# Kernel tuning notes

Measured on AMD Instinct MI355X. Metric: run time of the kernel, lower is better.

Reference implementation:

```python
import jax, jax.numpy as jnp
import numpy as np

EMBED_DIM = 1024
NUM_HEADS = 16
HEAD_DIM = EMBED_DIM // NUM_HEADS
SCALE = HEAD_DIM ** -0.5


def setup_inputs() -> dict:
    key = jax.random.key(0)
    ks = jax.random.split(key, 5)
    B, N, D = 2, 2048, EMBED_DIM
    std = D ** -0.5
    x = jax.random.normal(ks[0], (B, N, D), dtype=jnp.float32)
    W_qkv = jax.random.normal(ks[1], (D, 3 * D), dtype=jnp.float32) * std
    b_qkv = jnp.zeros((3 * D,), dtype=jnp.float32)
    W_proj = jax.random.normal(ks[2], (D, D), dtype=jnp.float32) * std
    b_proj = jnp.zeros((D,), dtype=jnp.float32)
    return {"x": x, "W_qkv": W_qkv, "b_qkv": b_qkv, "W_proj": W_proj, "b_proj": b_proj}


def reference(x, W_qkv, b_qkv, W_proj, b_proj):
    B, N, D = x.shape
    H, Hd = NUM_HEADS, HEAD_DIM
    qkv = x @ W_qkv + b_qkv                      # (B, N, 3D)
    qkv = qkv.reshape(B, N, 3, H, Hd)
    q = qkv[:, :, 0].transpose(0, 2, 1, 3)       # (B, H, N, Hd)
    k = qkv[:, :, 1].transpose(0, 2, 1, 3)
    v = qkv[:, :, 2].transpose(0, 2, 1, 3)
    attn = jnp.einsum('bhqd,bhkd->bhqk', q, k) * SCALE  # (B, H, N, N)
    attn = jax.nn.softmax(attn, axis=-1)
    out = jnp.einsum('bhqk,bhkd->bhqd', attn, v)        # (B, H, N, Hd)
    out = out.transpose(0, 2, 1, 3).reshape(B, N, D)
    return out @ W_proj + b_proj
```

## Files before the change

### kernel.cpp

```cpp
#include <hip/hip_runtime.h>
#include <stdint.h>

#define BATCH 2
#define NH 16
#define SEQ 2048
#define DIM 1024
#define HD 64
#define MROWS (BATCH*SEQ)

typedef __attribute__((ext_vector_type(8))) _Float16 f16x8;
typedef __attribute__((ext_vector_type(16))) float f32x16;
typedef __attribute__((ext_vector_type(4))) float f32x4;
typedef __attribute__((ext_vector_type(2))) __fp16 fp16x2;
typedef __attribute__((ext_vector_type(4))) short short4v;

__device__ __forceinline__ short f2h(float f) {
  union { _Float16 h; short s; } u;
  u.h = (_Float16)f;
  return u.s;
}

__device__ __forceinline__ float fast_exp2(float x) {
#if __has_builtin(__builtin_amdgcn_exp2f)
  return __builtin_amdgcn_exp2f(x);
#else
  return exp2f(x);
#endif
}

__device__ __forceinline__ unsigned pk2(float a, float b) {
  union { fp16x2 h; unsigned u; } x;
  x.h = __builtin_amdgcn_cvt_pkrtz(a, b);
  return x.u;
}

__device__ __forceinline__ void perm32swap(unsigned &a, unsigned &b) {
  unsigned as = (unsigned)__shfl_xor((int)a, 32);
  unsigned bs = (unsigned)__shfl_xor((int)b, 32);
  bool lo = ((threadIdx.x & 63) < 32);
  unsigned na = lo ? a : bs;
  unsigned nb = lo ? as : b;
  a = na; b = nb;
}

__device__ __forceinline__ void async_load16(const void* g, void* l) {
  __builtin_amdgcn_global_load_lds((const __attribute__((address_space(1))) void*)g,
                                   (__attribute__((address_space(3))) void*)l, 16, 0, 0);
}

__global__ __launch_bounds__(256) void k_cvt(const float* __restrict__ in,
                                             short* __restrict__ out, int n4) {
  int i = blockIdx.x * 256 + threadIdx.x;
  if (i >= n4) return;
  float4 v = ((const float4*)in)[i];
  short4v o;
  o[0] = f2h(v.x); o[1] = f2h(v.y); o[2] = f2h(v.z); o[3] = f2h(v.w);
  ((short4v*)out)[i] = o;
}

__global__ __launch_bounds__(256) void k_transpose(const float* __restrict__ in,
                                                   short* __restrict__ out,
                                                   int K, int N) {
  __shared__ float t[32][33];
  int n0 = blockIdx.x * 32, k0 = blockIdx.y * 32;
  int tx = threadIdx.x, ty = threadIdx.y;
  #pragma unroll
  for (int i = 0; i < 32; i += 8)
    t[ty + i][tx] = in[(size_t)(k0 + ty + i) * N + (n0 + tx)];
  __syncthreads();
  #pragma unroll
  for (int i = 0; i < 32; i += 8)
    out[(size_t)(n0 + ty + i) * K + (k0 + tx)] = f2h(t[tx][ty + i]);
}

template <int MODE>
__global__ __launch_bounds__(256) void k_gemm_bt(
    const short* __restrict__ A, const short* __restrict__ Bt,
    const float* __restrict__ bias,
    short* __restrict__ Qd, short* __restrict__ Kd, short* __restrict__ Vtd,
    float* __restrict__ Cf, int Ncols, int Kdim) {
  constexpr int BM = 128, BN = 128, BK = 32;
  __shared__ short Al[BM * BK];
  __shared__ short Bl[BN * BK];
  const int tid = threadIdx.x;
  const int lane = tid & 63;
  const int wid = tid >> 6;
  const int wr = wid >> 1, wc = wid & 1;
  const int m0 = blockIdx.y * BM, n0 = blockIdx.x * BN;
  const int l15 = lane & 15, lk = (lane >> 4) * 8;

  f32x4 acc[4][4] = {};

  for (int k0 = 0; k0 < Kdim; k0 += BK) {
    __syncthreads();
    #pragma unroll
    for (int i = 0; i < 2; i++) {
      int c = i * 256 + tid;
      async_load16(A + (size_t)(m0 + (c >> 2)) * Kdim + k0 + (c & 3) * 8, &Al[c * 8]);
    }
    #pragma unroll
    for (int i = 0; i < 2; i++) {
      int c = i * 256 + tid;
      async_load16(Bt + (size_t)(n0 + (c >> 2)) * Kdim + k0 + (c & 3) * 8, &Bl[c * 8]);
    }
    __syncthreads();

    f16x8 af[4], bfr[4];
    #pragma unroll
    for (int i = 0; i < 4; i++)
      af[i] = *(const f16x8*)&Al[(wr * 64 + i * 16 + l15) * BK + lk];
    #pragma unroll
    for (int j = 0; j < 4; j++)
      bfr[j] = *(const f16x8*)&Bl[(wc * 64 + j * 16 + l15) * BK + lk];
    #pragma unroll
    for (int i = 0; i < 4; i++)
      #pragma unroll
      for (int j = 0; j < 4; j++)
        acc[i][j] = __builtin_amdgcn_mfma_f32_16x16x32_f16(af[i], bfr[j], acc[i][j], 0, 0, 0);
  }

  const int rl = (lane >> 4) * 4;
  if (MODE == 0) {
    #pragma unroll
    for (int j = 0; j < 4; j++) {
      int col = n0 + wc * 64 + j * 16 + l15;
      float bv = bias[col];
      int sec = col >> 10;
      int cc = col & 1023;
      int h = cc >> 6, hd = cc & 63;
      float mul = (sec == 0) ? (0.125f * 1.44269504088896f) : 1.0f;
      #pragma unroll
      for (int i = 0; i < 4; i++) {
        int rowb = m0 + wr * 64 + i * 16 + rl;
        #pragma unroll
        for (int r = 0; r < 4; r++) {
          int row = rowb + r;
          int b = row >> 11, nr = row & 2047;
          short v = f2h((acc[i][j][r] + bv) * mul);
          size_t bh = (size_t)(b * NH + h);
          size_t base2 = bh * (size_t)(SEQ * HD);
          if (sec == 0) {
            Qd[base2 + (size_t)nr * HD + hd] = v;
          } else if (sec == 1) {
            Kd[base2 + (size_t)(((nr >> 5) * 4 + (hd >> 4)) * 512 +
                                (((hd >> 3) & 1) * 32 + (nr & 31)) * 8 + (hd & 7))] = v;
          } else {
            Vtd[base2 + (size_t)(((nr >> 4) * 2 + (hd >> 5)) * 512 +
                                 (((nr >> 3) & 1) * 32 + (hd & 31)) * 8 + (nr & 7))] = v;
          }
        }
      }
    }
  } else {
    #pragma unroll
    for (int j = 0; j < 4; j++) {
      int col = n0 + wc * 64 + j * 16 + l15;
      float bv = bias[col];
      #pragma unroll
      for (int i = 0; i < 4; i++) {
        int rowb = m0 + wr * 64 + i * 16 + rl;
        #pragma unroll
        for (int r = 0; r < 4; r++)
          Cf[(size_t)(rowb + r) * Ncols + col] = acc[i][j][r] + bv;
      }
    }
  }
}

#define QBLK 256
#define NKVT (SEQ / 64)

#define PACK8(sv, R0, lsv, OUT) do {                                        \
    float e0_ = fast_exp2((sv)[R0 + 0]), e1_ = fast_exp2((sv)[R0 + 1]);     \
    float e2_ = fast_exp2((sv)[R0 + 2]), e3_ = fast_exp2((sv)[R0 + 3]);     \
    float e4_ = fast_exp2((sv)[R0 + 4]), e5_ = fast_exp2((sv)[R0 + 5]);     \
    float e6_ = fast_exp2((sv)[R0 + 6]), e7_ = fast_exp2((sv)[R0 + 7]);     \
    lsv += ((e0_ + e1_) + (e2_ + e3_)) + ((e4_ + e5_) + (e6_ + e7_));       \
    unsigned u0_ = pk2(e0_, e1_), u1_ = pk2(e2_, e3_);                      \
    unsigned u2_ = pk2(e4_, e5_), u3_ = pk2(e6_, e7_);                      \
    perm32swap(u0_, u2_);                                                   \
    perm32swap(u1_, u3_);                                                   \
    union { unsigned u[4]; f16x8 v; } W_;                                   \
    W_.u[0] = u0_; W_.u[1] = u1_; W_.u[2] = u2_; W_.u[3] = u3_;             \
    OUT = W_.v;                                                             \
  } while (0)

__global__ __launch_bounds__(256) void k_flash(const short* __restrict__ Qd,
                                               const short* __restrict__ KB,
                                               const short* __restrict__ VB,
                                               short* __restrict__ Od) {
  __shared__ short Kl[2][4096];
  __shared__ short Vl[2][4096];
  const int tid = threadIdx.x;
  const int lane = tid & 63;
  const int w = tid >> 6;
  const int l31 = lane & 31, lh = lane >> 5;
  const int bh = blockIdx.x;
  const int q0 = blockIdx.y * QBLK + w * 64;
  const size_t base = (size_t)bh * (size_t)(SEQ * HD);

  f16x8 qf[2][4];
  #pragma unroll
  for (int qt = 0; qt < 2; qt++)
    #pragma unroll
    for (int ds = 0; ds < 4; ds++)
      qf[qt][ds] = *(const f16x8*)(Qd + base + (size_t)(q0 + qt * 32 + l31) * HD +
                                   ds * 16 + lh * 8);

  f32x16 o[2][2] = {};
  float lsum0 = 0.f, lsum1 = 0.f;

#define STAGE(kvt, buf) do {                                                \
    const short* ks_ = KB + base + (size_t)(kvt) * 4096;                    \
    const short* vs_ = VB + base + (size_t)(kvt) * 4096;                    \
    async_load16(ks_ + tid * 8, &Kl[buf][tid * 8]);                         \
    async_load16(ks_ + (tid + 256) * 8, &Kl[buf][(tid + 256) * 8]);         \
    async_load16(vs_ + tid * 8, &Vl[buf][tid * 8]);                         \
    async_load16(vs_ + (tid + 256) * 8, &Vl[buf][(tid + 256) * 8]);         \
  } while (0)

  auto compute = [&](int cur) {
    f16x8 p0[4], p1[4];
    {
      f16x8 kf[4];
      #pragma unroll
      for (int ds = 0; ds < 4; ds++)
        kf[ds] = *(const f16x8*)&Kl[cur][(ds * 64 + lane) * 8];
      f32x16 sA0 = {}, sA1 = {};
      #pragma unroll
      for (int ds = 0; ds < 4; ds++) {
        sA0 = __builtin_amdgcn_mfma_f32_32x32x16_f16(kf[ds], qf[0][ds], sA0, 0, 0, 0);
        sA1 = __builtin_amdgcn_mfma_f32_32x32x16_f16(kf[ds], qf[1][ds], sA1, 0, 0, 0);
      }
      PACK8(sA0, 0, lsum0, p0[0]); PACK8(sA0, 8, lsum0, p0[1]);
      PACK8(sA1, 0, lsum1, p1[0]); PACK8(sA1, 8, lsum1, p1[1]);
    }
    {
      f16x8 kf[4];
      #pragma unroll
      for (int ds = 0; ds < 4; ds++)
        kf[ds] = *(const f16x8*)&Kl[cur][((4 + ds) * 64 + lane) * 8];
      f32x16 sB0 = {}, sB1 = {};
      #pragma unroll
      for (int ds = 0; ds < 4; ds++) {
        sB0 = __builtin_amdgcn_mfma_f32_32x32x16_f16(kf[ds], qf[0][ds], sB0, 0, 0, 0);
        sB1 = __builtin_amdgcn_mfma_f32_32x32x16_f16(kf[ds], qf[1][ds], sB1, 0, 0, 0);
      }
      PACK8(sB0, 0, lsum0, p0[2]); PACK8(sB0, 8, lsum0, p0[3]);
      PACK8(sB1, 0, lsum1, p1[2]); PACK8(sB1, 8, lsum1, p1[3]);
    }
    f16x8 vf[4][2];
    #pragma unroll
    for (int ks = 0; ks < 4; ks++)
      #pragma unroll
      for (int hdt = 0; hdt < 2; hdt++)
        vf[ks][hdt] = *(const f16x8*)&Vl[cur][((ks * 2 + hdt) * 64 + lane) * 8];
    #pragma unroll
    for (int ks = 0; ks < 4; ks++) {
      o[0][0] = __builtin_amdgcn_mfma_f32_32x32x16_f16(p0[ks], vf[ks][0], o[0][0], 0, 0, 0);
      o[0][1] = __builtin_amdgcn_mfma_f32_32x32x16_f16(p0[ks], vf[ks][1], o[0][1], 0, 0, 0);
      o[1][0] = __builtin_amdgcn_mfma_f32_32x32x16_f16(p1[ks], vf[ks][0], o[1][0], 0, 0, 0);
      o[1][1] = __builtin_amdgcn_mfma_f32_32x32x16_f16(p1[ks], vf[ks][1], o[1][1], 0, 0, 0);
    }
  };

  STAGE(0, 0);
  __syncthreads();
  for (int kvt = 0; kvt < NKVT; kvt++) {
    int cur = kvt & 1;
    if (kvt + 1 < NKVT) STAGE(kvt + 1, cur ^ 1);
    compute(cur);
    __syncthreads();
  }
#undef STAGE

  lsum0 += __shfl_xor(lsum0, 32);
  lsum1 += __shfl_xor(lsum1, 32);
  float inv0 = 1.f / lsum0, inv1 = 1.f / lsum1;

  const int b = bh >> 4, h = bh & 15;
  #pragma unroll
  for (int reg = 0; reg < 16; reg++) {
    int qrow = (reg & 3) + 8 * (reg >> 2) + 4 * lh;
    float s0 = __shfl(inv0, qrow);
    float s1 = __shfl(inv1, qrow);
    size_t r0 = (size_t)(b * SEQ + q0 + qrow) * DIM + h * 64;
    size_t r1 = (size_t)(b * SEQ + q0 + 32 + qrow) * DIM + h * 64;
    Od[r0 + l31]      = f2h(o[0][0][reg] * s0);
    Od[r0 + 32 + l31] = f2h(o[0][1][reg] * s0);
    Od[r1 + l31]      = f2h(o[1][0][reg] * s1);
    Od[r1 + 32 + l31] = f2h(o[1][1][reg] * s1);
  }
}

extern "C" void kernel_launch(void* const* d_in, const int* in_sizes, int n_in,
                              void* d_out, int out_size, void* d_ws, size_t ws_size,
                              hipStream_t stream) {
  const float* x     = (const float*)d_in[0];
  const float* Wqkv  = (const float*)d_in[1];
  const float* bqkv  = (const float*)d_in[2];
  const float* Wproj = (const float*)d_in[3];
  const float* bproj = (const float*)d_in[4];
  float* out = (float*)d_out;

  char* ws = (char*)d_ws;
  short* x_h    = (short*)(ws);
  short* Wqkv_t = (short*)(ws + ((size_t)8  << 20));
  short* Wproj_t= (short*)(ws + ((size_t)14 << 20));
  short* Qd     = (short*)(ws + ((size_t)16 << 20));
  short* Kd     = (short*)(ws + ((size_t)24 << 20));
  short* Vtd    = (short*)(ws + ((size_t)32 << 20));
  short* Od     = (short*)(ws + ((size_t)40 << 20));

  k_cvt<<<(MROWS * DIM / 4 + 255) / 256, 256, 0, stream>>>(x, x_h, MROWS * DIM / 4);
  dim3 tb(32, 8);
  k_transpose<<<dim3(3 * DIM / 32, DIM / 32), tb, 0, stream>>>(Wqkv, Wqkv_t, DIM, 3 * DIM);
  k_transpose<<<dim3(DIM / 32, DIM / 32), tb, 0, stream>>>(Wproj, Wproj_t, DIM, DIM);
  k_gemm_bt<0><<<dim3(3 * DIM / 128, MROWS / 128), 256, 0, stream>>>(
      x_h, Wqkv_t, bqkv, Qd, Kd, Vtd, nullptr, 3 * DIM, DIM);
  k_flash<<<dim3(BATCH * NH, SEQ / QBLK), 256, 0, stream>>>(Qd, Kd, Vtd, Od);
  k_gemm_bt<1><<<dim3(DIM / 128, MROWS / 128), 256, 0, stream>>>(
      Od, Wproj_t, bproj, nullptr, nullptr, nullptr, out, DIM, DIM);
}
```

Measured before the change: 161.9 us.

## Halve flash query block per wave and hand-schedule async KV pipeline

Each wave now handles 32 query rows instead of 64 (QBLK 128), doubling the grid and cutting register use. The per-iteration __syncthreads is replaced by an explicit vmcnt wait, raw s_barrier and sched_barrier fences so the next tile's async loads stay in flight during compute. MFMA sections are wrapped in s_setprio. The aim is more occupancy and better load/compute overlap, at the cost of loading K/V tiles twice as often per query.

```diff
diff --git a/kernel.cpp b/kernel.cpp
--- a/kernel.cpp
+++ b/kernel.cpp
@@ -167,7 +167,7 @@
   }
 }
 
-#define QBLK 256
+#define QBLK 128
 #define NKVT (SEQ / 64)
 
 #define PACK8(sv, R0, lsv, OUT) do {                                        \
@@ -196,19 +196,16 @@
   const int w = tid >> 6;
   const int l31 = lane & 31, lh = lane >> 5;
   const int bh = blockIdx.x;
-  const int q0 = blockIdx.y * QBLK + w * 64;
+  const int q0 = blockIdx.y * QBLK + w * 32;
   const size_t base = (size_t)bh * (size_t)(SEQ * HD);
 
-  f16x8 qf[2][4];
+  f16x8 qf[4];
   #pragma unroll
-  for (int qt = 0; qt < 2; qt++)
-    #pragma unroll
-    for (int ds = 0; ds < 4; ds++)
-      qf[qt][ds] = *(const f16x8*)(Qd + base + (size_t)(q0 + qt * 32 + l31) * HD +
-                                   ds * 16 + lh * 8);
-
-  f32x16 o[2][2] = {};
-  float lsum0 = 0.f, lsum1 = 0.f;
+  for (int ds = 0; ds < 4; ds++)
+    qf[ds] = *(const f16x8*)(Qd + base + (size_t)(q0 + l31) * HD + ds * 16 + lh * 8);
+
+  f32x16 o[2] = {};
+  float lsum = 0.f;
 
 #define STAGE(kvt, buf) do {                                                \
     const short* ks_ = KB + base + (size_t)(kvt) * 4096;                    \
@@ -220,76 +217,66 @@
   } while (0)
 
   auto compute = [&](int cur) {
-    f16x8 p0[4], p1[4];
-    {
-      f16x8 kf[4];
-      #pragma unroll
-      for (int ds = 0; ds < 4; ds++)
-        kf[ds] = *(const f16x8*)&Kl[cur][(ds * 64 + lane) * 8];
-      f32x16 sA0 = {}, sA1 = {};
-      #pragma unroll
-      for (int ds = 0; ds < 4; ds++) {
-        sA0 = __builtin_amdgcn_mfma_f32_32x32x16_f16(kf[ds], qf[0][ds], sA0, 0, 0, 0);
-        sA1 = __builtin_amdgcn_mfma_f32_32x32x16_f16(kf[ds], qf[1][ds], sA1, 0, 0, 0);
-      }
-      PACK8(sA0, 0, lsum0, p0[0]); PACK8(sA0, 8, lsum0, p0[1]);
-      PACK8(sA1, 0, lsum1, p1[0]); PACK8(sA1, 8, lsum1, p1[1]);
-    }
-    {
-      f16x8 kf[4];
-      #pragma unroll
-      for (int ds = 0; ds < 4; ds++)
-        kf[ds] = *(const f16x8*)&Kl[cur][((4 + ds) * 64 + lane) * 8];
-      f32x16 sB0 = {}, sB1 = {};
-      #pragma unroll
-      for (int ds = 0; ds < 4; ds++) {
-        sB0 = __builtin_amdgcn_mfma_f32_32x32x16_f16(kf[ds], qf[0][ds], sB0, 0, 0, 0);
-        sB1 = __builtin_amdgcn_mfma_f32_32x32x16_f16(kf[ds], qf[1][ds], sB1, 0, 0, 0);
-      }
-      PACK8(sB0, 0, lsum0, p0[2]); PACK8(sB0, 8, lsum0, p0[3]);
-      PACK8(sB1, 0, lsum1, p1[2]); PACK8(sB1, 8, lsum1, p1[3]);
-    }
+    f16x8 kf0[4], kf1[4];
+    #pragma unroll
+    for (int ds = 0; ds < 4; ds++) {
+      kf0[ds] = *(const f16x8*)&Kl[cur][(ds * 64 + lane) * 8];
+      kf1[ds] = *(const f16x8*)&Kl[cur][((4 + ds) * 64 + lane) * 8];
+    }
+    f32x16 sA = {}, sB = {};
+    __builtin_amdgcn_s_setprio(1);
+    #pragma unroll
+    for (int ds = 0; ds < 4; ds++) {
+      sA = __builtin_amdgcn_mfma_f32_32x32x16_f16(kf0[ds], qf[ds], sA, 0, 0, 0);
+      sB = __builtin_amdgcn_mfma_f32_32x32x16_f16(kf1[ds], qf[ds], sB, 0, 0, 0);
+    }
+    __builtin_amdgcn_s_setprio(0);
     f16x8 vf[4][2];
     #pragma unroll
     for (int ks = 0; ks < 4; ks++)
       #pragma unroll
       for (int hdt = 0; hdt < 2; hdt++)
         vf[ks][hdt] = *(const f16x8*)&Vl[cur][((ks * 2 + hdt) * 64 + lane) * 8];
+    f16x8 p[4];
+    PACK8(sA, 0, lsum, p[0]); PACK8(sA, 8, lsum, p[1]);
+    PACK8(sB, 0, lsum, p[2]); PACK8(sB, 8, lsum, p[3]);
+    __builtin_amdgcn_s_setprio(1);
     #pragma unroll
     for (int ks = 0; ks < 4; ks++) {
-      o[0][0] = __builtin_amdgcn_mfma_f32_32x32x16_f16(p0[ks], vf[ks][0], o[0][0], 0, 0, 0);
-      o[0][1] = __builtin_amdgcn_mfma_f32_32x32x16_f16(p0[ks], vf[ks][1], o[0][1], 0, 0, 0);
-      o[1][0] = __builtin_amdgcn_mfma_f32_32x32x16_f16(p1[ks], vf[ks][0], o[1][0], 0, 0, 0);
-      o[1][1] = __builtin_amdgcn_mfma_f32_32x32x16_f16(p1[ks], vf[ks][1], o[1][1], 0, 0, 0);
-    }
+      o[0] = __builtin_amdgcn_mfma_f32_32x32x16_f16(p[ks], vf[ks][0], o[0], 0, 0, 0);
+      o[1] = __builtin_amdgcn_mfma_f32_32x32x16_f16(p[ks], vf[ks][1], o[1], 0, 0, 0);
+    }
+    __builtin_amdgcn_s_setprio(0);
   };
 
   STAGE(0, 0);
-  __syncthreads();
   for (int kvt = 0; kvt < NKVT; kvt++) {
     int cur = kvt & 1;
-    if (kvt + 1 < NKVT) STAGE(kvt + 1, cur ^ 1);
+    if (kvt + 1 < NKVT) {
+      STAGE(kvt + 1, cur ^ 1);
+      asm volatile("s_waitcnt vmcnt(4)" ::: "memory");
+    } else {
+      asm volatile("s_waitcnt vmcnt(0)" ::: "memory");
+    }
+    __builtin_amdgcn_s_barrier();
+    __builtin_amdgcn_sched_barrier(0);
     compute(cur);
-    __syncthreads();
+    __builtin_amdgcn_sched_barrier(0);
+    __builtin_amdgcn_s_barrier();
   }
 #undef STAGE
 
-  lsum0 += __shfl_xor(lsum0, 32);
-  lsum1 += __shfl_xor(lsum1, 32);
-  float inv0 = 1.f / lsum0, inv1 = 1.f / lsum1;
+  lsum += __shfl_xor(lsum, 32);
+  float inv = 1.f / lsum;
 
   const int b = bh >> 4, h = bh & 15;
   #pragma unroll
   for (int reg = 0; reg < 16; reg++) {
     int qrow = (reg & 3) + 8 * (reg >> 2) + 4 * lh;
-    float s0 = __shfl(inv0, qrow);
-    float s1 = __shfl(inv1, qrow);
+    float s = __shfl(inv, qrow);
     size_t r0 = (size_t)(b * SEQ + q0 + qrow) * DIM + h * 64;
-    size_t r1 = (size_t)(b * SEQ + q0 + 32 + qrow) * DIM + h * 64;
-    Od[r0 + l31]      = f2h(o[0][0][reg] * s0);
-    Od[r0 + 32 + l31] = f2h(o[0][1][reg] * s0);
-    Od[r1 + l31]      = f2h(o[1][0][reg] * s1);
-    Od[r1 + 32 + l31] = f2h(o[1][1][reg] * s1);
+    Od[r0 + l31]      = f2h(o[0][reg] * s);
+    Od[r0 + 32 + l31] = f2h(o[1][reg] * s);
   }
 }
 
```

Measured after the change: 153.8 us. 5.0% less time.
